# Kernel tuning notes

Measured on AMD Instinct MI355X. Metric: run time of the kernel, lower is better.

Reference implementation:

```python
import jax, jax.numpy as jnp
import numpy as np

EPS = 1e-5
NH = 8   # num_heads
P = 8    # patch_size (local window)

def layernorm(x, g, b):
    m = jnp.mean(x, axis=-1, keepdims=True)
    v = jnp.var(x, axis=-1, keepdims=True)
    return (x - m) * jax.lax.rsqrt(v + EPS) * g + b

def axis_embed(pos, nf):
    # DETR-style interleaved sin/cos along one axis -> (L, nf)
    dim_t = 10000.0 ** (2.0 * (jnp.arange(nf) // 2).astype(jnp.float32) / nf)
    p = pos[:, None] / dim_t
    return jnp.stack([jnp.sin(p[:, 0::2]), jnp.cos(p[:, 1::2])], axis=-1).reshape(pos.shape[0], nf)

def pos_embed_2d(E, H, W):
    # (H, W, E): first half of channels encode y, second half encode x
    half = E // 2
    ye = axis_embed(jnp.arange(1, H + 1, dtype=jnp.float32), half)
    xe = axis_embed(jnp.arange(1, W + 1, dtype=jnp.float32), half)
    return jnp.concatenate([jnp.broadcast_to(ye[:, None, :], (H, W, half)),
                            jnp.broadcast_to(xe[None, :, :], (H, W, half))], axis=-1)

def pos_embed_1d(L, E):
    # standard sinusoidal, (L, 1, E)
    pos = jnp.arange(L, dtype=jnp.float32)[:, None]
    div = jnp.exp(jnp.arange(0, E, 2, dtype=jnp.float32) * (-np.log(10000.0) / E))
    pe = jnp.zeros((L, E), jnp.float32)
    pe = pe.at[:, 0::2].set(jnp.sin(pos * div)).at[:, 1::2].set(jnp.cos(pos * div))
    return pe[:, None, :]

def mha(q, k, v, Wq, bq, Wk, bk, Wv, bv, Wo, bo, nh):
    # q,k,v: (B, L, C)
    B, Lq, C = q.shape
    hd = C // nh
    qh = (q @ Wq + bq).reshape(B, Lq, nh, hd)
    kh = (k @ Wk + bk).reshape(B, -1, nh, hd)
    vh = (v @ Wv + bv).reshape(B, -1, nh, hd)
    att = jax.nn.softmax(jnp.einsum('bqhd,bkhd->bhqk', qh, kh) / np.sqrt(hd).astype(np.float32), axis=-1)
    out = jnp.einsum('bhqk,bkhd->bqhd', att, vh).reshape(B, Lq, C)
    return out @ Wo + bo

def win_part(x):
    # (N,T,H,W,C) -> (N*T*nWin, P*P, C)
    N, T, H, W, C = x.shape
    x = x.reshape(N, T, H // P, P, W // P, P, C).transpose(0, 1, 2, 4, 3, 5, 6)
    return x.reshape(-1, P * P, C)

def forward(x, g1, b1, g2, b2, g3, b3, g4, b4,
            sWq, sbq, sWk, sbk, sWv, sbv, sWo, sbo,
            cW1, cb1, dwk, dwb, cW2, cb2,
            tWq, tbq, tWk, tbk, tWv, tbv, tWo, tbo,
            fW1, fb1, fW2, fb2):
    N, T, H, W, C = x.shape
    sl_pos = jnp.tile(pos_embed_2d(C, P, P), (H // P, W // P, 1))  # (H,W,C)
    tem_pos = pos_embed_1d(T, C)                                   # (T,1,C)

    # --- spatial local windowed MHSA (q=k=norm1(x+pos), v=norm1(x)) ---
    qk = win_part(layernorm(x + sl_pos, g1, b1))
    vv = win_part(layernorm(x, g1, b1))
    attn = mha(qk, qk, vv, sWq, sbq, sWk, sbk, sWv, sbv, sWo, sbo, NH)
    attn = attn.reshape(N, T, H // P, W // P, P, P, C).transpose(0, 1, 2, 4, 3, 5, 6).reshape(N, T, H, W, C)
    x = x + attn

    # --- Conv FFN: linear -> depthwise 3x3 -> GELU -> linear ---
    h = layernorm(x, g2, b2) @ cW1 + cb1
    Ch = h.shape[-1]
    h = h.reshape(N * T, H, W, Ch).transpose(0, 3, 1, 2)  # NCHW
    h = jax.lax.conv_general_dilated(h, dwk, (1, 1), 'SAME', feature_group_count=Ch,
                                     dimension_numbers=('NCHW', 'OIHW', 'NCHW')) + dwb[None, :, None, None]
    h = jax.nn.gelu(h, approximate=False)
    h = h.transpose(0, 2, 3, 1).reshape(N, T, H, W, Ch)
    x = x + (h @ cW2 + cb2)

    # --- temporal MHSA over T, tokens are (n,h,w) positions ---
    xt = x.transpose(1, 0, 2, 3, 4).reshape(T, N * H * W, C)
    xt = layernorm(xt, g3, b3)
    qt = layernorm(xt + tem_pos, g3, b3).transpose(1, 0, 2)  # (B,T,C)
    vt = layernorm(xt, g3, b3).transpose(1, 0, 2)
    xt = xt + mha(qt, qt, vt, tWq, tbq, tWk, tbk, tWv, tbv, tWo, tbo, NH).transpose(1, 0, 2)

    # --- FFN; original does x = x + drop3(x) (no residual, doubles output) ---
    xt = layernorm(xt, g4, b4)
    xt = jax.nn.gelu(xt @ fW1 + fb1, approximate=False) @ fW2 + fb2
    xt = xt + xt
    return xt.reshape(T, N, H, W, C).transpose(1, 0, 2, 3, 4)

def setup_inputs() -> dict:
    key = jax.random.key(0)
    N, T, H, W, C, DFF, HID = 4, 16, 32, 32, 256, 1024, 1024
    ks = iter(jax.random.split(key, 64))
    def w(*s):
        return jax.random.normal(next(ks), s, jnp.float32) * 0.02
    inp = dict(x=jax.random.normal(next(ks), (N, T, H, W, C), jnp.float32))
    for i in ('1', '2', '3', '4'):
        inp['g' + i] = jnp.ones((C,), jnp.float32)
        inp['b' + i] = jnp.zeros((C,), jnp.float32)
    for pfx in ('s', 't'):
        inp.update({pfx + 'Wq': w(C, C), pfx + 'bq': jnp.zeros((C,), jnp.float32),
                    pfx + 'Wk': w(C, C), pfx + 'bk': jnp.zeros((C,), jnp.float32),
                    pfx + 'Wv': w(C, C), pfx + 'bv': jnp.zeros((C,), jnp.float32),
                    pfx + 'Wo': w(C, C), pfx + 'bo': jnp.zeros((C,), jnp.float32)})
    inp.update(cW1=w(C, HID), cb1=jnp.zeros((HID,), jnp.float32),
               dwk=w(HID, 1, 3, 3), dwb=jnp.zeros((HID,), jnp.float32),
               cW2=w(HID, C), cb2=jnp.zeros((C,), jnp.float32))
    inp.update(fW1=w(C, DFF), fb1=jnp.zeros((DFF,), jnp.float32),
               fW2=w(DFF, C), fb2=jnp.zeros((C,), jnp.float32))
    return inp

def reference(x, g1, b1, g2, b2, g3, b3, g4, b4,
              sWq, sbq, sWk, sbk, sWv, sbv, sWo, sbo,
              cW1, cb1, dwk, dwb, cW2, cb2,
              tWq, tbq, tWk, tbk, tWv, tbv, tWo, tbo,
              fW1, fb1, fW2, fb2):
    return forward(x, g1, b1, g2, b2, g3, b3, g4, b4,
                   sWq, sbq, sWk, sbk, sWv, sbv, sWo, sbo,
                   cW1, cb1, dwk, dwb, cW2, cb2,
                   tWq, tbq, tWk, tbk, tWv, tbv, tWo, tbo,
                   fW1, fb1, fW2, fb2)
```

## Files before the change

kernel.cpp:

```cpp
#include <hip/hip_runtime.h>
#include <hip/hip_bf16.h>

typedef unsigned short u16;
typedef unsigned int u32;
typedef __attribute__((ext_vector_type(4))) float f32x4;
typedef __attribute__((ext_vector_type(8))) short s16x8;

static constexpr int Nn = 4, Tt = 16, Hh = 32, Ww = 32, Cc = 256;
static constexpr int Ltok = Nn * Tt * Hh * Ww;

__device__ __forceinline__ float bf2f(u16 v) {
  union { u32 u; float f; } t; t.u = ((u32)v) << 16; return t.f;
}
__device__ __forceinline__ u16 f2bf(float f) {
  union { u32 u; float f; } t; t.f = f;
  return (u16)((t.u + 0x7fffu + ((t.u >> 16) & 1u)) >> 16);
}
__device__ __forceinline__ ushort4 pack4(float a, float b, float c, float d) {
  ushort4 r; r.x = f2bf(a); r.y = f2bf(b); r.z = f2bf(c); r.w = f2bf(d); return r;
}
__device__ __forceinline__ float geluf(float x) {
  return 0.5f * x * (1.0f + erff(x * 0.70710678118654752f));
}
__device__ __forceinline__ float wsum(float v) {
#pragma unroll
  for (int o = 32; o > 0; o >>= 1) v += __shfl_xor(v, o, 64);
  return v;
}
__device__ __forceinline__ void ln_stats(float a0, float a1, float a2, float a3,
                                         float& m, float& inv) {
  float s  = wsum(a0 + a1 + a2 + a3);
  float s2 = wsum(a0 * a0 + a1 * a1 + a2 * a2 + a3 * a3);
  m = s * (1.0f / 256.0f);
  float v = s2 * (1.0f / 256.0f) - m * m;
  inv = rsqrtf(v + 1e-5f);
}
__device__ __forceinline__ void gload16(const u16* g, u16* l) {
  __builtin_amdgcn_global_load_lds(
      (const __attribute__((address_space(1))) void*)g,
      (__attribute__((address_space(3))) void*)l, 16, 0, 0);
}

__global__ __launch_bounds__(256) void k_pos(float* __restrict__ pe2d,
                                             float* __restrict__ pe1d,
                                             float* __restrict__ dwkT,
                                             float* __restrict__ zb,
                                             float* __restrict__ sqk,
                                             float* __restrict__ tqk,
                                             const float* __restrict__ dwk,
                                             const float* __restrict__ sbq,
                                             const float* __restrict__ sbk,
                                             const float* __restrict__ tbq,
                                             const float* __restrict__ tbk) {
  int idx = blockIdx.x * 256 + threadIdx.x;
  if (idx < 16384) {
    int y = idx >> 11, r = idx & 2047, x = r >> 8, c = r & 255;
    float pos; int cc;
    if (c < 128) { pos = (float)(y + 1); cc = c; }
    else         { pos = (float)(x + 1); cc = c - 128; }
    float e = (float)(cc & ~1) * (1.0f / 128.0f);
    float v = pos / powf(10000.0f, e);
    pe2d[idx] = (cc & 1) ? cosf(v) : sinf(v);
  } else if (idx < 20480) {
    int i = idx - 16384;
    int t = i >> 8, c = i & 255;
    float e = (float)(c & ~1) * (1.0f / 256.0f);
    float v = (float)t * powf(10000.0f, -e);
    pe1d[i] = (c & 1) ? cosf(v) : sinf(v);
  } else if (idx < 29696) {
    int i = idx - 20480;
    int c = i & 1023, tap = i >> 10;
    dwkT[tap * 1024 + c] = dwk[c * 9 + tap];
  } else if (idx < 30720) {
    zb[idx - 29696] = 0.0f;
  } else if (idx < 31232) {
    int i = idx - 30720;
    sqk[i] = (i < 256) ? sbq[i] : sbk[i - 256];
  } else if (idx < 31744) {
    int i = idx - 31232;
    tqk[i] = (i < 256) ? tbq[i] : tbk[i - 256];
  }
}

__global__ __launch_bounds__(256) void k_wprep(
    const float* __restrict__ s0, const float* __restrict__ s1,
    const float* __restrict__ s2, const float* __restrict__ s3,
    const float* __restrict__ s4, const float* __restrict__ s5,
    const float* __restrict__ s6, const float* __restrict__ s7,
    const float* __restrict__ cW1, const float* __restrict__ cW2,
    const float* __restrict__ fW1, const float* __restrict__ fW2,
    u16* __restrict__ WT) {
  __shared__ float Ls[32][33];
  int b = blockIdx.x;
// ... 52 lines not shown
  float m, inv;
  ln_stats(x0, x1, x2, x3, m, inv);
  float4 gv = *(const float4*)&g[c0];
  float4 bv = *(const float4*)&b[c0];
  *(ushort4*)&out[(size_t)l * Cc + c0] =
      pack4((x0 - m) * inv * gv.x + bv.x, (x1 - m) * inv * gv.y + bv.y,
            (x2 - m) * inv * gv.z + bv.z, (x3 - m) * inv * gv.w + bv.w);
}

__global__ __launch_bounds__(256) void k_ln3b(const u16* __restrict__ xa,
                                              const float* __restrict__ g,
                                              const float* __restrict__ b,
                                              const float* __restrict__ pe1d,
                                              u16* __restrict__ xt_base,
                                              u16* __restrict__ qt,
                                              u16* __restrict__ vt) {
  int l = blockIdx.x * 4 + (threadIdx.x >> 6);
  int lane = threadIdx.x & 63, c0 = lane * 4;
  ushort4 xv4 = *(const ushort4*)&xa[(size_t)l * Cc + c0];
  float x0 = bf2f(xv4.x), x1 = bf2f(xv4.y), x2 = bf2f(xv4.z), x3 = bf2f(xv4.w);
  float4 gv = *(const float4*)&g[c0];
  float4 bv = *(const float4*)&b[c0];
  float m, inv;
  ln_stats(x0, x1, x2, x3, m, inv);
  float t0 = (x0 - m) * inv * gv.x + bv.x;
  float t1 = (x1 - m) * inv * gv.y + bv.y;
  float t2 = (x2 - m) * inv * gv.z + bv.z;
  float t3 = (x3 - m) * inv * gv.w + bv.w;
  *(ushort4*)&xt_base[(size_t)l * Cc + c0] = pack4(t0, t1, t2, t3);
  float m2, inv2;
  ln_stats(t0, t1, t2, t3, m2, inv2);
  *(ushort4*)&vt[(size_t)l * Cc + c0] =
      pack4((t0 - m2) * inv2 * gv.x + bv.x, (t1 - m2) * inv2 * gv.y + bv.y,
            (t2 - m2) * inv2 * gv.z + bv.z, (t3 - m2) * inv2 * gv.w + bv.w);
  int tt = (l >> 10) & 15;
  float4 pv = *(const float4*)&pe1d[tt * Cc + c0];
  float s0 = t0 + pv.x, s1 = t1 + pv.y, s2 = t2 + pv.z, s3 = t3 + pv.w;
  float m3, inv3;
  ln_stats(s0, s1, s2, s3, m3, inv3);
  *(ushort4*)&qt[(size_t)l * Cc + c0] =
      pack4((s0 - m3) * inv3 * gv.x + bv.x, (s1 - m3) * inv3 * gv.y + bv.y,
            (s2 - m3) * inv3 * gv.z + bv.z, (s3 - m3) * inv3 * gv.w + bv.w);
}

template <int MODE>
__global__ __launch_bounds__(256, 2) void k_sgemm(const u16* __restrict__ A,
                                                  const u16* __restrict__ WT,
                                                  int wt_stride,
                                                  const float* __restrict__ bias,
                                                  int bias_stride,
                                                  const void* __restrict__ res,
                                                  void* __restrict__ out,
                                                  size_t out_xoff, int ldout) {
  __shared__ u16 SMEM[24576];
  const int tid = threadIdx.x;
  const int wave = tid >> 6, lane = tid & 63;
  const int fr = lane & 15, fs = lane >> 4;
  const int bx = blockIdx.x;
  const int r0base = blockIdx.y * 128;
  WT += (size_t)bx * wt_stride;
  bias += bx * bias_stride;
  u16* ob = (u16*)out + (size_t)bx * out_xoff;
  s16x8 wreg[4][8];
#pragma unroll
  for (int ni = 0; ni < 4; ++ni)
#pragma unroll
    for (int kt = 0; kt < 8; ++kt)
      wreg[ni][kt] = *(const s16x8*)&WT[(size_t)(wave * 64 + ni * 16 + fr) * 256 +
                                        kt * 32 + fs * 8];
  auto stage = [&](int buf, int r0) {
    u16* Ad = SMEM + buf * 8192;
#pragma unroll
    for (int i = 0; i < 4; ++i) {
      int idx = i * 256 + tid;
      int row = idx >> 5, s = idx & 31;
      gload16(A + (size_t)(r0 + row) * 256 + ((s ^ row) << 3), &Ad[idx * 8]);
    }
  };
  u16* sc = SMEM + 16384 + wave * 2048;
  stage(0, r0base);
  __syncthreads();
#pragma unroll 1
  for (int c = 0; c < 4; ++c) {
    if (c < 3) stage((c + 1) & 1, r0base + (c + 1) * 32);
    const u16* As = SMEM + (c & 1) * 8192;
    f32x4 acc[2][4] = {};
#pragma unroll
    for (int kt = 0; kt < 8; ++kt) {
      s16x8 a0 = *(const s16x8*)&As[(fr * 32 + ((kt * 4 + fs) ^ fr)) * 8];
      s16x8 a1 = *(const s16x8*)&As[((16 + fr) * 32 + ((kt * 4 + fs) ^ (16 + fr))) * 8];
#pragma unroll
      for (int ni = 0; ni < 4; ++ni) {
        acc[0][ni] = __builtin_amdgcn_mfma_f32_16x16x32_bf16(a0, wreg[ni][kt],
                                                             acc[0][ni], 0, 0, 0);
        acc[1][ni] = __builtin_amdgcn_mfma_f32_16x16x32_bf16(a1, wreg[ni][kt],
                                                             acc[1][ni], 0, 0, 0);
      }
    }
    const int r0 = r0base + c * 32;
    if constexpr (MODE == 5) {
      u16* o = (u16*)out;
#pragma unroll
      for (int ni = 0; ni < 4; ++ni) {
        int gc = wave * 64 + ni * 16 + fr;
        float bv = bias[gc];
#pragma unroll
        for (int mi = 0; mi < 2; ++mi) {
          int gr = r0 + mi * 16 + fs * 4;
          *(ushort4*)&o[(size_t)gc * (size_t)Ltok + gr] =
              pack4(acc[mi][ni][0] + bv, acc[mi][ni][1] + bv,
                    acc[mi][ni][2] + bv, acc[mi][ni][3] + bv);
        }
      }
    } else {
#pragma unroll
      for (int ni = 0; ni < 4; ++ni) {
        float bv = bias[wave * 64 + ni * 16 + fr];
#pragma unroll
        for (int mi = 0; mi < 2; ++mi)
#pragma unroll
          for (int r = 0; r < 4; ++r) {
            int row = mi * 16 + fs * 4 + r;
            int col = ni * 16 + fr;
            float v = acc[mi][ni][r] + bv;
            if constexpr (MODE == 1) v = geluf(v);
            sc[row * 64 + (col ^ ((row & 3) << 3))] = f2bf(v);
          }
      }
#pragma unroll
      for (int p = 0; p < 4; ++p) {
        int row = p * 8 + (lane >> 3);
        int c8 = (lane & 7) * 8;
        ushort4 u0 = *(const ushort4*)&sc[row * 64 + ((c8 ^ ((row & 3) << 3)))];
        ushort4 u1 = *(const ushort4*)&sc[row * 64 + (((c8 + 4) ^ ((row & 3) << 3)))];
        int gr = r0 + row;
        int gc = wave * 64 + c8;
        size_t o = (size_t)gr * (size_t)ldout + gc;
        if constexpr (MODE == 3) {
          const u16* rp = (const u16*)res;
          ushort4 r0v = *(const ushort4*)&rp[(size_t)gr * 256 + gc];
          ushort4 r1v = *(const ushort4*)&rp[(size_t)gr * 256 + gc + 4];
          u0 = pack4(bf2f(u0.x) + bf2f(r0v.x), bf2f(u0.y) + bf2f(r0v.y),
                     bf2f(u0.z) + bf2f(r0v.z), bf2f(u0.w) + bf2f(r0v.w));
          u1 = pack4(bf2f(u1.x) + bf2f(r1v.x), bf2f(u1.y) + bf2f(r1v.y),
                     bf2f(u1.z) + bf2f(r1v.z), bf2f(u1.w) + bf2f(r1v.w));
        }
        if constexpr (MODE == 7) {
          const float* rp = (const float*)res;
          float4 r0v = *(const float4*)&rp[(size_t)gr * 256 + gc];
          float4 r1v = *(const float4*)&rp[(size_t)gr * 256 + gc + 4];
          u0 = pack4(bf2f(u0.x) + r0v.x, bf2f(u0.y) + r0v.y,
                     bf2f(u0.z) + r0v.z, bf2f(u0.w) + r0v.w);
          u1 = pack4(bf2f(u1.x) + r1v.x, bf2f(u1.y) + r1v.y,
                     bf2f(u1.z) + r1v.z, bf2f(u1.w) + r1v.w);
        }
        *(ushort4*)&ob[o] = u0;
        *(ushort4*)&ob[o + 4] = u1;
      }
    }
    __syncthreads();
  }
}

__global__ __launch_bounds__(256, 2) void k_cgemm(const u16* __restrict__ A,
                                                  const u16* __restrict__ WT,
                                                  const float* __restrict__ bias,
                                                  u16* __restrict__ xa) {
  __shared__ u16 SMEM[18432];
  const int tid = threadIdx.x;
  const int wave = tid >> 6, lane = tid & 63;
  const int fr = lane & 15, fs = lane >> 4;
  const int bx = blockIdx.x;
  const int r0base = blockIdx.y * 128;
  s16x8 wreg[2][16];
#pragma unroll
  for (int ni = 0; ni < 2; ++ni)
#pragma unroll
    for (int kt = 0; kt < 16; ++kt)
      wreg[ni][kt] = *(const s16x8*)&WT[(size_t)(bx * 128 + wave * 32 + ni * 16 + fr) *
                                            1024 + kt * 32 + fs * 8];
  auto stage = [&](int buf, int r0) {
    u16* Ad = SMEM + buf * 8192;
#pragma unroll
    for (int i = 0; i < 4; ++i) {
      int idx = i * 256 + tid;
      int row = idx >> 6, s = idx & 63;
      gload16(A + (size_t)(r0 + row) * 512 + ((s ^ (row & 7)) << 3), &Ad[idx * 8]);
    }
  };
  u16* sc = SMEM + 16384 + wave * 512;
  stage(0, r0base);
  __syncthreads();
#pragma unroll 1
  for (int c = 0; c < 8; ++c) {
    if (c < 7) stage((c + 1) & 1, r0base + (c + 1) * 16);
    const u16* As = SMEM + (c & 1) * 8192;
    f32x4 acc[2] = {};
#pragma unroll
    for (int kt = 0; kt < 16; ++kt) {
      s16x8 a = *(const s16x8*)&As[fr * 512 + (((kt * 4 + fs) ^ (fr & 7)) << 3)];
#pragma unroll
      for (int ni = 0; ni < 2; ++ni)
        acc[ni] = __builtin_amdgcn_mfma_f32_16x16x32_bf16(a, wreg[ni][kt],
                                                          acc[ni], 0, 0, 0);
    }
    const int r0 = r0base + c * 16;
#pragma unroll
    for (int ni = 0; ni < 2; ++ni) {
      float bv = bias[bx * 128 + wave * 32 + ni * 16 + fr];
#pragma unroll
      for (int r = 0; r < 4; ++r) {
        int row = fs * 4 + r;
        int col = ni * 16 + fr;
        sc[row * 32 + (col ^ ((row & 3) << 3))] = f2bf(acc[ni][r] + bv);
      }
    }
    {
      int row = lane >> 2, c8 = (lane & 3) * 8;
      ushort4 u0 = *(const ushort4*)&sc[row * 32 + (c8 ^ ((row & 3) << 3))];
      ushort4 u1 = *(const ushort4*)&sc[row * 32 + ((c8 + 4) ^ ((row & 3) << 3))];
      int gr = r0 + row;
      int gc = bx * 128 + wave * 32 + c8;
      size_t o = (size_t)gr * 256 + gc;
      ushort4 r0v = *(const ushort4*)&xa[o];
      ushort4 r1v = *(const ushort4*)&xa[o + 4];
      *(ushort4*)&xa[o] = pack4(bf2f(u0.x) + bf2f(r0v.x), bf2f(u0.y) + bf2f(r0v.y),
                                bf2f(u0.z) + bf2f(r0v.z), bf2f(u0.w) + bf2f(r0v.w));
      *(ushort4*)&xa[o + 4] = pack4(bf2f(u1.x) + bf2f(r1v.x), bf2f(u1.y) + bf2f(r1v.y),
                                    bf2f(u1.z) + bf2f(r1v.z), bf2f(u1.w) + bf2f(r1v.w));
    }
    __syncthreads();
  }
}

__global__ __launch_bounds__(256, 2) void k_fgemm(const u16* __restrict__ A,
                                                  const u16* __restrict__ WT,
                                                  const float* __restrict__ bias,
                                                  float* __restrict__ out) {
  __shared__ u16 SMEM[34816];
  const int tid = threadIdx.x;
  const int wave = tid >> 6, lane = tid & 63;
  const int fr = lane & 15, fs = lane >> 4;
  const int bx = blockIdx.x;
  const int r0base = blockIdx.y * 128;
  const int col = bx * 64 + wave * 16 + fr;
  s16x8 wreg[32];
#pragma unroll
  for (int kt = 0; kt < 32; ++kt)
    wreg[kt] = *(const s16x8*)&WT[(size_t)col * 1024 + kt * 32 + fs * 8];
  auto stage = [&](int buf, int r0) {
    u16* Ad = SMEM + buf * 16384;
#pragma unroll
    for (int i = 0; i < 8; ++i) {
      int idx = i * 256 + tid;
      int row = idx >> 7, s = idx & 127;
      gload16(A + (size_t)(r0 + row) * 1024 + ((s ^ (row & 7)) << 3), &Ad[idx * 8]);
    }
  };
  float* scf = (float*)(SMEM + 32768) + wave * 256;
  stage(0, r0base);
  __syncthreads();
#pragma unroll 1
  for (int c = 0; c < 8; ++c) {
    if (c < 7) stage((c + 1) & 1, r0base + (c + 1) * 16);
    const u16* As = SMEM + (c & 1) * 16384;
    f32x4 acc = {};
#pragma unroll
    for (int kt = 0; kt < 32; ++kt) {
      s16x8 a = *(const s16x8*)&As[fr * 1024 + (((kt * 4 + fs) ^ (fr & 7)) << 3)];
      acc = __builtin_amdgcn_mfma_f32_16x16x32_bf16(a, wreg[kt], acc, 0, 0, 0);
    }
    const int r0 = r0base + c * 16;
    {
      float bv = bias[col];
#pragma unroll
      for (int r = 0; r < 4; ++r) {
        int row = fs * 4 + r;
        scf[row * 16 + (fr ^ ((row & 3) << 2))] = 2.0f * (acc[r] + bv);
      }
    }
    {
      int row = lane >> 2, c4 = (lane & 3) * 4;
      f32x4 v4 = *(const f32x4*)&scf[row * 16 + (c4 ^ ((row & 3) << 2))];
      int gr = r0 + row;
      *(float4*)&out[(size_t)gr * 256 + bx * 64 + wave * 16 + c4] =
          make_float4(v4[0], v4[1], v4[2], v4[3]);
    }
    __syncthreads();
  }
}

__global__ __launch_bounds__(256) void k_sattn2(const u16* __restrict__ Q,
                                                const u16* __restrict__ Kb,
                                                const u16* __restrict__ VT,
                                                u16* __restrict__ ctx) {
  __shared__ u16 P_lds[4][4096];
  const int tid = threadIdx.x;
  const int wave = tid >> 6, lane = tid & 63;
  const int fr = lane & 15, fs = lane >> 4;
  const int wi = blockIdx.x >> 1;
  const int head = (blockIdx.x & 1) * 4 + wave;
  const int ft = wi >> 4, wy = (wi >> 2) & 3, wx = wi & 3;
  const int base = ft * 1024 + wy * 256 + wx * 8;
  const float scale = 0.17677669529663688f;
  const int ch = head * 32 + fs * 8;
  s16x8 ka[4], qb[4];
#pragma unroll
  for (int t4 = 0; t4 < 4; ++t4) {
    int tok = base + (2 * t4 + (fr >> 3)) * 32 + (fr & 7);
    ka[t4] = *(const s16x8*)&Kb[(size_t)tok * 256 + ch];
    qb[t4] = *(const s16x8*)&Q[(size_t)tok * 256 + ch];
  }
  f32x4 s[4][4] = {};
#pragma unroll
  for (int kt = 0; kt < 4; ++kt)
#pragma unroll
    for (int qt = 0; qt < 4; ++qt)
      s[kt][qt] = __builtin_amdgcn_mfma_f32_16x16x32_bf16(ka[kt], qb[qt], s[kt][qt], 0, 0, 0);
  u16* pw = P_lds[wave];
#pragma unroll
  for (int qt = 0; qt < 4; ++qt) {
    float m = -1e30f;
#pragma unroll
    for (int kt = 0; kt < 4; ++kt)
#pragma unroll
      for (int r = 0; r < 4; ++r) m = fmaxf(m, s[kt][qt][r]);
    m = fmaxf(m, __shfl_xor(m, 16, 64));
    m = fmaxf(m, __shfl_xor(m, 32, 64));
    m *= scale;
    float e[4][4];
    float sum = 0.f;
#pragma unroll
    for (int kt = 0; kt < 4; ++kt)
#pragma unroll
      for (int r = 0; r < 4; ++r) {
        e[kt][r] = __expf(s[kt][qt][r] * scale - m);
        sum += e[kt][r];
      }
    sum += __shfl_xor(sum, 16, 64);
    sum += __shfl_xor(sum, 32, 64);
    float il = 1.0f / sum;
// ... 123 lines not shown
      const u16* hp = (const u16*)&hv;
      int tap = (ky + 1) * 3 + (kx + 1);
      float wk[8];
      *(float4*)&wk[0] = *(const float4*)&dwkT[tap * 1024 + tc0];
      *(float4*)&wk[4] = *(const float4*)&dwkT[tap * 1024 + tc0 + 4];
#pragma unroll
      for (int u = 0; u < 8; ++u) acc[u] = fmaf(bf2f(hp[u]), wk[u], acc[u]);
    }
  }
  size_t ob = (size_t)l * 512 + oco + c0;
  *(ushort4*)&Hout[ob] = pack4(geluf(acc[0]), geluf(acc[1]), geluf(acc[2]), geluf(acc[3]));
  *(ushort4*)&Hout[ob + 4] = pack4(geluf(acc[4]), geluf(acc[5]), geluf(acc[6]), geluf(acc[7]));
}

extern "C" void kernel_launch(void* const* d_in, const int* in_sizes, int n_in,
                              void* d_out, int out_size, void* d_ws, size_t ws_size,
                              hipStream_t stream) {
  (void)in_sizes; (void)n_in; (void)out_size; (void)ws_size;
  const float* x   = (const float*)d_in[0];
  const float* g1  = (const float*)d_in[1];  const float* b1  = (const float*)d_in[2];
  const float* g2  = (const float*)d_in[3];  const float* b2  = (const float*)d_in[4];
  const float* g3  = (const float*)d_in[5];  const float* b3  = (const float*)d_in[6];
  const float* g4  = (const float*)d_in[7];  const float* b4  = (const float*)d_in[8];
  const float* sWq = (const float*)d_in[9];  const float* sbq = (const float*)d_in[10];
  const float* sWk = (const float*)d_in[11]; const float* sbk = (const float*)d_in[12];
  const float* sWv = (const float*)d_in[13]; const float* sbv = (const float*)d_in[14];
  const float* sWo = (const float*)d_in[15]; const float* sbo = (const float*)d_in[16];
  const float* tWq = (const float*)d_in[17]; const float* tbq = (const float*)d_in[18];
  const float* tWk = (const float*)d_in[19]; const float* tbk = (const float*)d_in[20];
  const float* tWv = (const float*)d_in[21]; const float* tbv = (const float*)d_in[22];
  const float* tWo = (const float*)d_in[23]; const float* tbo = (const float*)d_in[24];
  const float* cW1 = (const float*)d_in[25]; const float* cb1 = (const float*)d_in[26];
  const float* dwk = (const float*)d_in[27]; const float* dwb = (const float*)d_in[28];
  const float* cW2 = (const float*)d_in[29]; const float* cb2 = (const float*)d_in[30];
  const float* fW1 = (const float*)d_in[31]; const float* fb1 = (const float*)d_in[32];
  const float* fW2 = (const float*)d_in[33]; const float* fb2 = (const float*)d_in[34];

  char* ws = (char*)d_ws;
  const size_t MB = 1ull << 20;
  float* PE2D = (float*)(ws);
  float* PE1D = (float*)(ws + (64 << 10));
  float* DWKT = (float*)(ws + (80 << 10));
  float* ZB   = (float*)(ws + (116 << 10));
  float* SQK  = (float*)(ws + (120 << 10));
  float* TQK  = (float*)(ws + (122 << 10));
  u16*   WT   = (u16*)(ws + (128 << 10));
  u16* XA  = (u16*)(ws + 4 * MB);
  u16* X1  = (u16*)(ws + 4 * MB);
  u16* H1A = (u16*)(ws + 36 * MB);
  u16* B1  = (u16*)(ws + 68 * MB);
  u16* B2  = (u16*)(ws + 100 * MB);
  u16* B3  = (u16*)(ws + 132 * MB);
  u16* B4  = (u16*)(ws + 164 * MB);
  u16* H1B = B4;
  u16* H2h = B2;
  u16* F1  = (u16*)(ws + 4 * MB);

  u16* sWqT = WT;
  u16* sWvT = WT + 2 * 65536;   u16* sWoT = WT + 3 * 65536;
  u16* tWqT = WT + 4 * 65536;
  u16* tWvT = WT + 6 * 65536;   u16* tWoT = WT + 7 * 65536;
  u16* cW1T = WT + 524288;      u16* cW2T = WT + 786432;
  u16* fW1T = WT + 1048576;     u16* fW2T = WT + 1310720;

  dim3 blk(256);
  dim3 gLN(Ltok / 4);

  k_pos<<<dim3(124), blk, 0, stream>>>(PE2D, PE1D, DWKT, ZB, SQK, TQK,
                                       dwk, sbq, sbk, tbq, tbk);
  k_wprep<<<dim3(1536), blk, 0, stream>>>(sWq, sWk, sWv, sWo, tWq, tWk, tWv, tWo,
                                          cW1, cW2, fW1, fW2, WT);
  k_ln1<<<gLN, blk, 0, stream>>>(x, g1, b1, PE2D, B1, B2);
  k_sgemm<5><<<dim3(1, 512), blk, 0, stream>>>(B2, sWvT, 0, sbv, 0, nullptr,
                                               B3, 0, 0);
  k_sgemm<0><<<dim3(2, 512), blk, 0, stream>>>(B1, sWqT, 65536, SQK, 256, nullptr,
                                               B2, 33554432ull, 256);
  k_sattn2<<<dim3(2048), blk, 0, stream>>>(B2, B4, B3, B1);
  k_sgemm<7><<<dim3(1, 512), blk, 0, stream>>>(B1, sWoT, 0, sbo, 0, x,
                                               XA, 0, 256);
  k_lnb<<<gLN, blk, 0, stream>>>(XA, g2, b2, B1);
  for (int h = 0; h < 2; ++h) {
    k_sgemm<0><<<dim3(2, 512), blk, 0, stream>>>(B1, cW1T + h * 2 * 65536, 65536,
                                                 cb1 + h * 512, 256, nullptr,
                                                 H1A, 67108864ull, 256);
    k_dwconv<<<dim3(Ltok * 32 / 256), blk, 0, stream>>>(H1A, DWKT, dwb,
                                                        (h * 2) * 256, 0, H2h);
    k_dwconv<<<dim3(Ltok * 32 / 256), blk, 0, stream>>>(H1B, DWKT, dwb,
                                                        (h * 2 + 1) * 256, 256, H2h);
    k_cgemm<<<dim3(2, 512), blk, 0, stream>>>(H2h, cW2T + h * 512,
                                              h ? cb2 : ZB, XA);
  }
  k_ln3b<<<gLN, blk, 0, stream>>>(XA, g3, b3, PE1D, B1, B2, B3);
  k_sgemm<0><<<dim3(1, 512), blk, 0, stream>>>(B3, tWvT, 0, tbv, 0, nullptr,
                                               B4, 0, 256);
  k_sgemm<0><<<dim3(2, 512), blk, 0, stream>>>(B2, tWqT, 65536, TQK, 256, nullptr,
                                               X1, 67108864ull, 256);
  k_tattn2<<<dim3(4096), blk, 0, stream>>>(X1, B3, B4, B2);
  k_sgemm<3><<<dim3(1, 512), blk, 0, stream>>>(B2, tWoT, 0, tbo, 0, B1,
                                               B3, 0, 256);
  k_lnb<<<gLN, blk, 0, stream>>>(B3, g4, b4, B4);
  k_sgemm<1><<<dim3(4, 512), blk, 0, stream>>>(B4, fW1T, 65536, fb1, 256, nullptr,
                                               F1, 256ull, 1024);
  k_fgemm<<<dim3(4, 512), blk, 0, stream>>>(F1, fW2T, fb2, (float*)d_out);
}
```

Measured before the change: 794.6 us.

## Load GEMM A-fragments directly from global into registers instead of LDS staging

The three GEMM kernels (k_sgemm, k_cgemm, k_fgemm) stop staging A tiles into shared memory with global_load_lds and block-wide barriers. Each wave now loads its 16-row A fragments straight into registers, ping-ponging between two register buffers so the next tile's loads overlap the current tile's MFMAs. The only shared memory left is a small per-wave scratch for the output transpose. k_cgemm is also retiled to 64 output columns per block, doubling its grid. This removes LDS traffic and __syncthreads, but each wave now fetches the same rows redundantly from global/L2, and register pressure rises, which may hurt occupancy.

```diff
diff --git a/kernel.cpp b/kernel.cpp
--- a/kernel.cpp
+++ b/kernel.cpp
@@ -34,11 +34,6 @@
   m = s * (1.0f / 256.0f);
   float v = s2 * (1.0f / 256.0f) - m * m;
   inv = rsqrtf(v + 1e-5f);
-}
-__device__ __forceinline__ void gload16(const u16* g, u16* l) {
-  __builtin_amdgcn_global_load_lds(
-      (const __attribute__((address_space(1))) void*)g,
-      (__attribute__((address_space(3))) void*)l, 16, 0, 0);
 }
 
 __global__ __launch_bounds__(256) void k_pos(float* __restrict__ pe2d,
@@ -197,7 +192,7 @@
                                                   const void* __restrict__ res,
                                                   void* __restrict__ out,
                                                   size_t out_xoff, int ldout) {
-  __shared__ u16 SMEM[24576];
+  __shared__ u16 SC[4][1024];
   const int tid = threadIdx.x;
   const int wave = tid >> 6, lane = tid & 63;
   const int fr = lane & 15, fs = lane >> 4;
@@ -213,97 +208,88 @@
     for (int kt = 0; kt < 8; ++kt)
       wreg[ni][kt] = *(const s16x8*)&WT[(size_t)(wave * 64 + ni * 16 + fr) * 256 +
                                         kt * 32 + fs * 8];
-  auto stage = [&](int buf, int r0) {
-    u16* Ad = SMEM + buf * 8192;
-#pragma unroll
-    for (int i = 0; i < 4; ++i) {
-      int idx = i * 256 + tid;
-      int row = idx >> 5, s = idx & 31;
-      gload16(A + (size_t)(r0 + row) * 256 + ((s ^ row) << 3), &Ad[idx * 8]);
-    }
+  const u16* Arow = A + (size_t)(r0base + fr) * 256 + fs * 8;
+  u16* sc = SC[wave];
+
+  s16x8 afA[8], afB[8];
+  auto lda = [&](s16x8* af, int t) {
+#pragma unroll
+    for (int kt = 0; kt < 8; ++kt)
+      af[kt] = *(const s16x8*)(Arow + t * 4096 + kt * 32);
   };
-  u16* sc = SMEM + 16384 + wave * 2048;
-  stage(0, r0base);
-  __syncthreads();
-#pragma unroll 1
-  for (int c = 0; c < 4; ++c) {
-    if (c < 3) stage((c + 1) & 1, r0base + (c + 1) * 32);
-    const u16* As = SMEM + (c & 1) * 8192;
-    f32x4 acc[2][4] = {};
-#pragma unroll
-    for (int kt = 0; kt < 8; ++kt) {
-      s16x8 a0 = *(const s16x8*)&As[(fr * 32 + ((kt * 4 + fs) ^ fr)) * 8];
-      s16x8 a1 = *(const s16x8*)&As[((16 + fr) * 32 + ((kt * 4 + fs) ^ (16 + fr))) * 8];
-#pragma unroll
-      for (int ni = 0; ni < 4; ++ni) {
-        acc[0][ni] = __builtin_amdgcn_mfma_f32_16x16x32_bf16(a0, wreg[ni][kt],
-                                                             acc[0][ni], 0, 0, 0);
-        acc[1][ni] = __builtin_amdgcn_mfma_f32_16x16x32_bf16(a1, wreg[ni][kt],
-                                                             acc[1][ni], 0, 0, 0);
-      }
-    }
-    const int r0 = r0base + c * 32;
+  auto work = [&](const s16x8* af, int t) {
+    f32x4 acc[4] = {};
+#pragma unroll
+    for (int kt = 0; kt < 8; ++kt)
+#pragma unroll
+      for (int ni = 0; ni < 4; ++ni)
+        acc[ni] = __builtin_amdgcn_mfma_f32_16x16x32_bf16(af[kt], wreg[ni][kt],
+                                                          acc[ni], 0, 0, 0);
+    const int r0 = r0base + t * 16;
     if constexpr (MODE == 5) {
       u16* o = (u16*)out;
 #pragma unroll
       for (int ni = 0; ni < 4; ++ni) {
         int gc = wave * 64 + ni * 16 + fr;
         float bv = bias[gc];
-#pragma unroll
-        for (int mi = 0; mi < 2; ++mi) {
-          int gr = r0 + mi * 16 + fs * 4;
-          *(ushort4*)&o[(size_t)gc * (size_t)Ltok + gr] =
-              pack4(acc[mi][ni][0] + bv, acc[mi][ni][1] + bv,
-                    acc[mi][ni][2] + bv, acc[mi][ni][3] + bv);
-        }
+        int gr = r0 + fs * 4;
+        *(ushort4*)&o[(size_t)gc * (size_t)Ltok + gr] =
+            pack4(acc[ni][0] + bv, acc[ni][1] + bv, acc[ni][2] + bv, acc[ni][3] + bv);
       }
-    } else {
-#pragma unroll
-      for (int ni = 0; ni < 4; ++ni) {
-        float bv = bias[wave * 64 + ni * 16 + fr];
-#pragma unroll
-        for (int mi = 0; mi < 2; ++mi)
-#pragma unroll
-          for (int r = 0; r < 4; ++r) {
-            int row = mi * 16 + fs * 4 + r;
-            int col = ni * 16 + fr;
-            float v = acc[mi][ni][r] + bv;
-            if constexpr (MODE == 1) v = geluf(v);
-            sc[row * 64 + (col ^ ((row & 3) << 3))] = f2bf(v);
-          }
+      return;
+    }
+#pragma unroll
+    for (int ni = 0; ni < 4; ++ni) {
+      float bv = bias[wave * 64 + ni * 16 + fr];
+#pragma unroll
+      for (int r = 0; r < 4; ++r) {
+        int row = fs * 4 + r;
+        int col = ni * 16 + fr;
+        float v = acc[ni][r] + bv;
+        if constexpr (MODE == 1) v = geluf(v);
+        sc[row * 64 + (col ^ ((row & 3) << 3))] = f2bf(v);
       }
-#pragma unroll
-      for (int p = 0; p < 4; ++p) {
-        int row = p * 8 + (lane >> 3);
-        int c8 = (lane & 7) * 8;
-        ushort4 u0 = *(const ushort4*)&sc[row * 64 + ((c8 ^ ((row & 3) << 3)))];
-        ushort4 u1 = *(const ushort4*)&sc[row * 64 + (((c8 + 4) ^ ((row & 3) << 3)))];
-        int gr = r0 + row;
-        int gc = wave * 64 + c8;
-        size_t o = (size_t)gr * (size_t)ldout + gc;
-        if constexpr (MODE == 3) {
-          const u16* rp = (const u16*)res;
-          ushort4 r0v = *(const ushort4*)&rp[(size_t)gr * 256 + gc];
-          ushort4 r1v = *(const ushort4*)&rp[(size_t)gr * 256 + gc + 4];
-          u0 = pack4(bf2f(u0.x) + bf2f(r0v.x), bf2f(u0.y) + bf2f(r0v.y),
-                     bf2f(u0.z) + bf2f(r0v.z), bf2f(u0.w) + bf2f(r0v.w));
-          u1 = pack4(bf2f(u1.x) + bf2f(r1v.x), bf2f(u1.y) + bf2f(r1v.y),
-                     bf2f(u1.z) + bf2f(r1v.z), bf2f(u1.w) + bf2f(r1v.w));
-        }
-        if constexpr (MODE == 7) {
-          const float* rp = (const float*)res;
-          float4 r0v = *(const float4*)&rp[(size_t)gr * 256 + gc];
-          float4 r1v = *(const float4*)&rp[(size_t)gr * 256 + gc + 4];
-          u0 = pack4(bf2f(u0.x) + r0v.x, bf2f(u0.y) + r0v.y,
-                     bf2f(u0.z) + r0v.z, bf2f(u0.w) + r0v.w);
-          u1 = pack4(bf2f(u1.x) + r1v.x, bf2f(u1.y) + r1v.y,
-                     bf2f(u1.z) + r1v.z, bf2f(u1.w) + r1v.w);
-        }
-        *(ushort4*)&ob[o] = u0;
-        *(ushort4*)&ob[o + 4] = u1;
+    }
+#pragma unroll
+    for (int p = 0; p < 2; ++p) {
+      int row = p * 8 + (lane >> 3);
+      int c8 = (lane & 7) * 8;
+      uint4 u = *(const uint4*)&sc[row * 64 + (c8 ^ ((row & 3) << 3))];
+      int gr = r0 + row;
+      int gc = wave * 64 + c8;
+      size_t o = (size_t)gr * (size_t)ldout + gc;
+      if constexpr (MODE == 3) {
+        uint4 rv = *(const uint4*)&((const u16*)res)[(size_t)gr * 256 + gc];
+        const u16* up = (const u16*)&u;
+        const u16* rp = (const u16*)&rv;
+        u16 ov[8];
+#pragma unroll
+        for (int j = 0; j < 8; ++j) ov[j] = f2bf(bf2f(up[j]) + bf2f(rp[j]));
+        u = *(const uint4*)ov;
       }
-    }
-    __syncthreads();
+      if constexpr (MODE == 7) {
+        const float* rp = (const float*)res;
+        float4 r0v = *(const float4*)&rp[(size_t)gr * 256 + gc];
+        float4 r1v = *(const float4*)&rp[(size_t)gr * 256 + gc + 4];
+        const u16* up = (const u16*)&u;
+        u16 ov[8];
+        ov[0] = f2bf(bf2f(up[0]) + r0v.x); ov[1] = f2bf(bf2f(up[1]) + r0v.y);
+        ov[2] = f2bf(bf2f(up[2]) + r0v.z); ov[3] = f2bf(bf2f(up[3]) + r0v.w);
+        ov[4] = f2bf(bf2f(up[4]) + r1v.x); ov[5] = f2bf(bf2f(up[5]) + r1v.y);
+        ov[6] = f2bf(bf2f(up[6]) + r1v.z); ov[7] = f2bf(bf2f(up[7]) + r1v.w);
+        u = *(const uint4*)ov;
+      }
+      *(uint4*)&ob[o] = u;
+    }
+  };
+
+  lda(afA, 0);
+#pragma unroll
+  for (int tp = 0; tp < 4; ++tp) {
+    lda(afB, tp * 2 + 1);
+    work(afA, tp * 2);
+    if (tp < 3) lda(afA, tp * 2 + 2);
+    work(afB, tp * 2 + 1);
   }
 }
 
@@ -311,70 +297,57 @@
                                                   const u16* __restrict__ WT,
                                                   const float* __restrict__ bias,
                                                   u16* __restrict__ xa) {
-  __shared__ u16 SMEM[18432];
+  __shared__ u16 SC[4][256];
   const int tid = threadIdx.x;
   const int wave = tid >> 6, lane = tid & 63;
   const int fr = lane & 15, fs = lane >> 4;
   const int bx = blockIdx.x;
   const int r0base = blockIdx.y * 128;
-  s16x8 wreg[2][16];
-#pragma unroll
-  for (int ni = 0; ni < 2; ++ni)
+  const int col = bx * 64 + wave * 16 + fr;
+  s16x8 wreg[16];
+#pragma unroll
+  for (int kt = 0; kt < 16; ++kt)
+    wreg[kt] = *(const s16x8*)&WT[(size_t)col * 1024 + kt * 32 + fs * 8];
+  const u16* Arow = A + (size_t)(r0base + fr) * 512 + fs * 8;
+  u16* sc = SC[wave];
+  const float bv = bias[col];
+
+  s16x8 afA[16], afB[16];
+  auto lda = [&](s16x8* af, int t) {
 #pragma unroll
     for (int kt = 0; kt < 16; ++kt)
-      wreg[ni][kt] = *(const s16x8*)&WT[(size_t)(bx * 128 + wave * 32 + ni * 16 + fr) *
-                                            1024 + kt * 32 + fs * 8];
-  auto stage = [&](int buf, int r0) {
-    u16* Ad = SMEM + buf * 8192;
-#pragma unroll
-    for (int i = 0; i < 4; ++i) {
-      int idx = i * 256 + tid;
-      int row = idx >> 6, s = idx & 63;
-      gload16(A + (size_t)(r0 + row) * 512 + ((s ^ (row & 7)) << 3), &Ad[idx * 8]);
-    }
+      af[kt] = *(const s16x8*)(Arow + t * 8192 + kt * 32);
   };
-  u16* sc = SMEM + 16384 + wave * 512;
-  stage(0, r0base);
-  __syncthreads();
-#pragma unroll 1
-  for (int c = 0; c < 8; ++c) {
-    if (c < 7) stage((c + 1) & 1, r0base + (c + 1) * 16);
-    const u16* As = SMEM + (c & 1) * 8192;
-    f32x4 acc[2] = {};
-#pragma unroll
-    for (int kt = 0; kt < 16; ++kt) {
-      s16x8 a = *(const s16x8*)&As[fr * 512 + (((kt * 4 + fs) ^ (fr & 7)) << 3)];
-#pragma unroll
-      for (int ni = 0; ni < 2; ++ni)
-        acc[ni] = __builtin_amdgcn_mfma_f32_16x16x32_bf16(a, wreg[ni][kt],
-                                                          acc[ni], 0, 0, 0);
-    }
-    const int r0 = r0base + c * 16;
-#pragma unroll
-    for (int ni = 0; ni < 2; ++ni) {
-      float bv = bias[bx * 128 + wave * 32 + ni * 16 + fr];
-#pragma unroll
-      for (int r = 0; r < 4; ++r) {
-        int row = fs * 4 + r;
-        int col = ni * 16 + fr;
-        sc[row * 32 + (col ^ ((row & 3) << 3))] = f2bf(acc[ni][r] + bv);
-      }
+  auto work = [&](const s16x8* af, int t) {
+    f32x4 acc = {};
+#pragma unroll
+    for (int kt = 0; kt < 16; ++kt)
+      acc = __builtin_amdgcn_mfma_f32_16x16x32_bf16(af[kt], wreg[kt], acc, 0, 0, 0);
+    const int r0 = r0base + t * 16;
+#pragma unroll
+    for (int r = 0; r < 4; ++r) {
+      int row = fs * 4 + r;
+      sc[row * 16 + (fr ^ (((row >> 2) & 3) << 2))] = f2bf(acc[r] + bv);
     }
     {
-      int row = lane >> 2, c8 = (lane & 3) * 8;
-      ushort4 u0 = *(const ushort4*)&sc[row * 32 + (c8 ^ ((row & 3) << 3))];
-      ushort4 u1 = *(const ushort4*)&sc[row * 32 + ((c8 + 4) ^ ((row & 3) << 3))];
+      int row = lane >> 2, c4 = (lane & 3) * 4;
+      ushort4 u = *(const ushort4*)&sc[row * 16 + (c4 ^ (((row >> 2) & 3) << 2))];
       int gr = r0 + row;
-      int gc = bx * 128 + wave * 32 + c8;
+      int gc = bx * 64 + wave * 16 + c4;
       size_t o = (size_t)gr * 256 + gc;
-      ushort4 r0v = *(const ushort4*)&xa[o];
-      ushort4 r1v = *(const ushort4*)&xa[o + 4];
-      *(ushort4*)&xa[o] = pack4(bf2f(u0.x) + bf2f(r0v.x), bf2f(u0.y) + bf2f(r0v.y),
-                                bf2f(u0.z) + bf2f(r0v.z), bf2f(u0.w) + bf2f(r0v.w));
-      *(ushort4*)&xa[o + 4] = pack4(bf2f(u1.x) + bf2f(r1v.x), bf2f(u1.y) + bf2f(r1v.y),
-                                    bf2f(u1.z) + bf2f(r1v.z), bf2f(u1.w) + bf2f(r1v.w));
-    }
-    __syncthreads();
+      ushort4 rv = *(const ushort4*)&xa[o];
+      *(ushort4*)&xa[o] = pack4(bf2f(u.x) + bf2f(rv.x), bf2f(u.y) + bf2f(rv.y),
+                                bf2f(u.z) + bf2f(rv.z), bf2f(u.w) + bf2f(rv.w));
+    }
+  };
+
+  lda(afA, 0);
+#pragma unroll
+  for (int tp = 0; tp < 4; ++tp) {
+    lda(afB, tp * 2 + 1);
+    work(afA, tp * 2);
+    if (tp < 3) lda(afA, tp * 2 + 2);
+    work(afB, tp * 2 + 1);
   }
 }
 
@@ -382,7 +355,7 @@
                                                   const u16* __restrict__ WT,
                                                   const float* __restrict__ bias,
                                                   float* __restrict__ out) {
-  __shared__ u16 SMEM[34816];
+  __shared__ float SCF[4][256];
   const int tid = threadIdx.x;
   const int wave = tid >> 6, lane = tid & 63;
   const int fr = lane & 15, fs = lane >> 4;
@@ -393,45 +366,44 @@
 #pragma unroll
   for (int kt = 0; kt < 32; ++kt)
     wreg[kt] = *(const s16x8*)&WT[(size_t)col * 1024 + kt * 32 + fs * 8];
-  auto stage = [&](int buf, int r0) {
-    u16* Ad = SMEM + buf * 16384;
-#pragma unroll
-    for (int i = 0; i < 8; ++i) {
-      int idx = i * 256 + tid;
-      int row = idx >> 7, s = idx & 127;
-      gload16(A + (size_t)(r0 + row) * 1024 + ((s ^ (row & 7)) << 3), &Ad[idx * 8]);
-    }
+  const u16* Arow = A + (size_t)(r0base + fr) * 1024 + fs * 8;
+  float* sc = SCF[wave];
+  const float bv = bias[col];
+
+  s16x8 aA[8], aB[8];
+  auto ld8 = [&](s16x8* af, int t, int h) {
+#pragma unroll
+    for (int kt = 0; kt < 8; ++kt)
+      af[kt] = *(const s16x8*)(Arow + t * 16384 + (h * 8 + kt) * 32);
   };
-  float* scf = (float*)(SMEM + 32768) + wave * 256;
-  stage(0, r0base);
-  __syncthreads();
-#pragma unroll 1
-  for (int c = 0; c < 8; ++c) {
-    if (c < 7) stage((c + 1) & 1, r0base + (c + 1) * 16);
-    const u16* As = SMEM + (c & 1) * 16384;
+  auto m8 = [&](const s16x8* af, int h, f32x4& acc) {
+#pragma unroll
+    for (int kt = 0; kt < 8; ++kt)
+      acc = __builtin_amdgcn_mfma_f32_16x16x32_bf16(af[kt], wreg[h * 8 + kt],
+                                                    acc, 0, 0, 0);
+  };
+
+  ld8(aA, 0, 0);
+  for (int t = 0; t < 8; ++t) {
     f32x4 acc = {};
-#pragma unroll
-    for (int kt = 0; kt < 32; ++kt) {
-      s16x8 a = *(const s16x8*)&As[fr * 1024 + (((kt * 4 + fs) ^ (fr & 7)) << 3)];
-      acc = __builtin_amdgcn_mfma_f32_16x16x32_bf16(a, wreg[kt], acc, 0, 0, 0);
-    }
-    const int r0 = r0base + c * 16;
-    {
-      float bv = bias[col];
-#pragma unroll
-      for (int r = 0; r < 4; ++r) {
-        int row = fs * 4 + r;
-        scf[row * 16 + (fr ^ ((row & 3) << 2))] = 2.0f * (acc[r] + bv);
-      }
+    ld8(aB, t, 1); m8(aA, 0, acc);
+    ld8(aA, t, 2); m8(aB, 1, acc);
+    ld8(aB, t, 3); m8(aA, 2, acc);
+    if (t < 7) ld8(aA, t + 1, 0);
+    m8(aB, 3, acc);
+    const int r0 = r0base + t * 16;
+#pragma unroll
+    for (int r = 0; r < 4; ++r) {
+      int row = fs * 4 + r;
+      sc[row * 16 + (fr ^ (((row >> 2) & 3) << 2))] = 2.0f * (acc[r] + bv);
     }
     {
       int row = lane >> 2, c4 = (lane & 3) * 4;
-      f32x4 v4 = *(const f32x4*)&scf[row * 16 + (c4 ^ ((row & 3) << 2))];
+      f32x4 v4 = *(const f32x4*)&sc[row * 16 + (c4 ^ (((row >> 2) & 3) << 2))];
       int gr = r0 + row;
       *(float4*)&out[(size_t)gr * 256 + bx * 64 + wave * 16 + c4] =
           make_float4(v4[0], v4[1], v4[2], v4[3]);
     }
-    __syncthreads();
   }
 }
 
@@ -661,7 +633,6 @@
   u16* B2  = (u16*)(ws + 100 * MB);
   u16* B3  = (u16*)(ws + 132 * MB);
   u16* B4  = (u16*)(ws + 164 * MB);
-  u16* H1B = B4;
   u16* H2h = B2;
   u16* F1  = (u16*)(ws + 4 * MB);
 
@@ -694,9 +665,9 @@
                                                  H1A, 67108864ull, 256);
     k_dwconv<<<dim3(Ltok * 32 / 256), blk, 0, stream>>>(H1A, DWKT, dwb,
                                                         (h * 2) * 256, 0, H2h);
-    k_dwconv<<<dim3(Ltok * 32 / 256), blk, 0, stream>>>(H1B, DWKT, dwb,
+    k_dwconv<<<dim3(Ltok * 32 / 256), blk, 0, stream>>>(B4, DWKT, dwb,
                                                         (h * 2 + 1) * 256, 256, H2h);
-    k_cgemm<<<dim3(2, 512), blk, 0, stream>>>(H2h, cW2T + h * 512,
+    k_cgemm<<<dim3(4, 512), blk, 0, stream>>>(H2h, cW2T + h * 512,
                                               h ? cb2 : ZB, XA);
   }
   k_ln3b<<<gLN, blk, 0, stream>>>(XA, g3, b3, PE1D, B1, B2, B3);
```

Result: slower. 1.395 ms (+75.6%).

## Halve rows per GEMM block and split fgemm K staging to cut LDS use

Applied to the files above, without the earlier changes.

Each GEMM block now handles 64 rows instead of 128, and the grids double to 1024 row-blocks, giving more blocks to fill the GPU and shorter per-block tails. The FFN2 GEMM now stages A in half-K chunks of 512 columns with a persistent accumulator, which shrinks its shared-memory footprint from about 68 KB. The cgemm and fgemm swizzles change to a full-row XOR. The trade-off is that each block reloads its register-resident weights over fewer rows, so weight-load overhead per row doubles.

```diff
diff --git a/kernel.cpp b/kernel.cpp
--- a/kernel.cpp
+++ b/kernel.cpp
@@ -202,7 +202,7 @@
   const int wave = tid >> 6, lane = tid & 63;
   const int fr = lane & 15, fs = lane >> 4;
   const int bx = blockIdx.x;
-  const int r0base = blockIdx.y * 128;
+  const int r0base = blockIdx.y * 64;
   WT += (size_t)bx * wt_stride;
   bias += bx * bias_stride;
   u16* ob = (u16*)out + (size_t)bx * out_xoff;
@@ -213,21 +213,22 @@
     for (int kt = 0; kt < 8; ++kt)
       wreg[ni][kt] = *(const s16x8*)&WT[(size_t)(wave * 64 + ni * 16 + fr) * 256 +
                                         kt * 32 + fs * 8];
-  auto stage = [&](int buf, int r0) {
+  auto stage = [&](int buf, int c) {
     u16* Ad = SMEM + buf * 8192;
 #pragma unroll
     for (int i = 0; i < 4; ++i) {
       int idx = i * 256 + tid;
       int row = idx >> 5, s = idx & 31;
-      gload16(A + (size_t)(r0 + row) * 256 + ((s ^ row) << 3), &Ad[idx * 8]);
+      gload16(A + (size_t)(r0base + c * 32 + row) * 256 + ((s ^ row) << 3),
+              &Ad[idx * 8]);
     }
   };
   u16* sc = SMEM + 16384 + wave * 2048;
-  stage(0, r0base);
+  stage(0, 0);
   __syncthreads();
 #pragma unroll 1
-  for (int c = 0; c < 4; ++c) {
-    if (c < 3) stage((c + 1) & 1, r0base + (c + 1) * 32);
+  for (int c = 0; c < 2; ++c) {
+    if (c < 1) stage(1, 1);
     const u16* As = SMEM + (c & 1) * 8192;
     f32x4 acc[2][4] = {};
 #pragma unroll
@@ -316,7 +317,7 @@
   const int wave = tid >> 6, lane = tid & 63;
   const int fr = lane & 15, fs = lane >> 4;
   const int bx = blockIdx.x;
-  const int r0base = blockIdx.y * 128;
+  const int r0base = blockIdx.y * 64;
   s16x8 wreg[2][16];
 #pragma unroll
   for (int ni = 0; ni < 2; ++ni)
@@ -324,26 +325,27 @@
     for (int kt = 0; kt < 16; ++kt)
       wreg[ni][kt] = *(const s16x8*)&WT[(size_t)(bx * 128 + wave * 32 + ni * 16 + fr) *
                                             1024 + kt * 32 + fs * 8];
-  auto stage = [&](int buf, int r0) {
+  auto stage = [&](int buf, int c) {
     u16* Ad = SMEM + buf * 8192;
 #pragma unroll
     for (int i = 0; i < 4; ++i) {
       int idx = i * 256 + tid;
       int row = idx >> 6, s = idx & 63;
-      gload16(A + (size_t)(r0 + row) * 512 + ((s ^ (row & 7)) << 3), &Ad[idx * 8]);
+      gload16(A + (size_t)(r0base + c * 16 + row) * 512 + ((s ^ row) << 3),
+              &Ad[idx * 8]);
     }
   };
   u16* sc = SMEM + 16384 + wave * 512;
-  stage(0, r0base);
+  stage(0, 0);
   __syncthreads();
 #pragma unroll 1
-  for (int c = 0; c < 8; ++c) {
-    if (c < 7) stage((c + 1) & 1, r0base + (c + 1) * 16);
+  for (int c = 0; c < 4; ++c) {
+    if (c < 3) stage((c + 1) & 1, c + 1);
     const u16* As = SMEM + (c & 1) * 8192;
     f32x4 acc[2] = {};
 #pragma unroll
     for (int kt = 0; kt < 16; ++kt) {
-      s16x8 a = *(const s16x8*)&As[fr * 512 + (((kt * 4 + fs) ^ (fr & 7)) << 3)];
+      s16x8 a = *(const s16x8*)&As[(fr * 64 + ((kt * 4 + fs) ^ fr)) * 8];
 #pragma unroll
       for (int ni = 0; ni < 2; ++ni)
         acc[ni] = __builtin_amdgcn_mfma_f32_16x16x32_bf16(a, wreg[ni][kt],
@@ -382,54 +384,59 @@
                                                   const u16* __restrict__ WT,
                                                   const float* __restrict__ bias,
                                                   float* __restrict__ out) {
-  __shared__ u16 SMEM[34816];
+  __shared__ u16 AB[2][8192];
+  __shared__ float SCF[4][256];
   const int tid = threadIdx.x;
   const int wave = tid >> 6, lane = tid & 63;
   const int fr = lane & 15, fs = lane >> 4;
   const int bx = blockIdx.x;
-  const int r0base = blockIdx.y * 128;
+  const int r0base = blockIdx.y * 64;
   const int col = bx * 64 + wave * 16 + fr;
   s16x8 wreg[32];
 #pragma unroll
   for (int kt = 0; kt < 32; ++kt)
     wreg[kt] = *(const s16x8*)&WT[(size_t)col * 1024 + kt * 32 + fs * 8];
-  auto stage = [&](int buf, int r0) {
-    u16* Ad = SMEM + buf * 16384;
-#pragma unroll
-    for (int i = 0; i < 8; ++i) {
+  const float bv = bias[col];
+  float* sc = SCF[wave];
+
+  auto stage = [&](int buf, int s) {
+    int t = s >> 1, h = s & 1;
+#pragma unroll
+    for (int i = 0; i < 4; ++i) {
       int idx = i * 256 + tid;
-      int row = idx >> 7, s = idx & 127;
-      gload16(A + (size_t)(r0 + row) * 1024 + ((s ^ (row & 7)) << 3), &Ad[idx * 8]);
+      int row = idx >> 6, ss = idx & 63;
+      gload16(A + (size_t)(r0base + t * 16 + row) * 1024 + h * 512 + ((ss ^ row) << 3),
+              &AB[buf][idx * 8]);
     }
   };
-  float* scf = (float*)(SMEM + 32768) + wave * 256;
-  stage(0, r0base);
+  stage(0, 0);
   __syncthreads();
+  f32x4 acc = {};
 #pragma unroll 1
-  for (int c = 0; c < 8; ++c) {
-    if (c < 7) stage((c + 1) & 1, r0base + (c + 1) * 16);
-    const u16* As = SMEM + (c & 1) * 16384;
-    f32x4 acc = {};
-#pragma unroll
-    for (int kt = 0; kt < 32; ++kt) {
-      s16x8 a = *(const s16x8*)&As[fr * 1024 + (((kt * 4 + fs) ^ (fr & 7)) << 3)];
-      acc = __builtin_amdgcn_mfma_f32_16x16x32_bf16(a, wreg[kt], acc, 0, 0, 0);
-    }
-    const int r0 = r0base + c * 16;
-    {
-      float bv = bias[col];
+  for (int s = 0; s < 8; ++s) {
+    if (s < 7) stage((s + 1) & 1, s + 1);
+    const u16* As = AB[s & 1];
+    const int h = s & 1;
+#pragma unroll
+    for (int kt = 0; kt < 16; ++kt) {
+      s16x8 a = *(const s16x8*)&As[(fr * 64 + ((kt * 4 + fs) ^ fr)) * 8];
+      acc = __builtin_amdgcn_mfma_f32_16x16x32_bf16(a, wreg[h * 16 + kt], acc, 0, 0, 0);
+    }
+    if (h) {
+      const int r0 = r0base + (s >> 1) * 16;
 #pragma unroll
       for (int r = 0; r < 4; ++r) {
         int row = fs * 4 + r;
-        scf[row * 16 + (fr ^ ((row & 3) << 2))] = 2.0f * (acc[r] + bv);
-      }
-    }
-    {
-      int row = lane >> 2, c4 = (lane & 3) * 4;
-      f32x4 v4 = *(const f32x4*)&scf[row * 16 + (c4 ^ ((row & 3) << 2))];
-      int gr = r0 + row;
-      *(float4*)&out[(size_t)gr * 256 + bx * 64 + wave * 16 + c4] =
-          make_float4(v4[0], v4[1], v4[2], v4[3]);
+        sc[row * 16 + (fr ^ ((row & 3) << 2))] = 2.0f * (acc[r] + bv);
+      }
+      {
+        int row = lane >> 2, c4 = (lane & 3) * 4;
+        f32x4 v4 = *(const f32x4*)&sc[row * 16 + (c4 ^ ((row & 3) << 2))];
+        int gr = r0 + row;
+        *(float4*)&out[(size_t)gr * 256 + bx * 64 + wave * 16 + c4] =
+            make_float4(v4[0], v4[1], v4[2], v4[3]);
+      }
+      acc = f32x4{0.f, 0.f, 0.f, 0.f};
     }
     __syncthreads();
   }
@@ -661,7 +668,6 @@
   u16* B2  = (u16*)(ws + 100 * MB);
   u16* B3  = (u16*)(ws + 132 * MB);
   u16* B4  = (u16*)(ws + 164 * MB);
-  u16* H1B = B4;
   u16* H2h = B2;
   u16* F1  = (u16*)(ws + 4 * MB);
 
@@ -680,35 +686,35 @@
   k_wprep<<<dim3(1536), blk, 0, stream>>>(sWq, sWk, sWv, sWo, tWq, tWk, tWv, tWo,
                                           cW1, cW2, fW1, fW2, WT);
   k_ln1<<<gLN, blk, 0, stream>>>(x, g1, b1, PE2D, B1, B2);
-  k_sgemm<5><<<dim3(1, 512), blk, 0, stream>>>(B2, sWvT, 0, sbv, 0, nullptr,
-                                               B3, 0, 0);
-  k_sgemm<0><<<dim3(2, 512), blk, 0, stream>>>(B1, sWqT, 65536, SQK, 256, nullptr,
-                                               B2, 33554432ull, 256);
+  k_sgemm<5><<<dim3(1, 1024), blk, 0, stream>>>(B2, sWvT, 0, sbv, 0, nullptr,
+                                                B3, 0, 0);
+  k_sgemm<0><<<dim3(2, 1024), blk, 0, stream>>>(B1, sWqT, 65536, SQK, 256, nullptr,
+                                                B2, 33554432ull, 256);
   k_sattn2<<<dim3(2048), blk, 0, stream>>>(B2, B4, B3, B1);
-  k_sgemm<7><<<dim3(1, 512), blk, 0, stream>>>(B1, sWoT, 0, sbo, 0, x,
-                                               XA, 0, 256);
+  k_sgemm<7><<<dim3(1, 1024), blk, 0, stream>>>(B1, sWoT, 0, sbo, 0, x,
+                                                XA, 0, 256);
   k_lnb<<<gLN, blk, 0, stream>>>(XA, g2, b2, B1);
   for (int h = 0; h < 2; ++h) {
-    k_sgemm<0><<<dim3(2, 512), blk, 0, stream>>>(B1, cW1T + h * 2 * 65536, 65536,
-                                                 cb1 + h * 512, 256, nullptr,
-                                                 H1A, 67108864ull, 256);
+    k_sgemm<0><<<dim3(2, 1024), blk, 0, stream>>>(B1, cW1T + h * 2 * 65536, 65536,
+                                                  cb1 + h * 512, 256, nullptr,
+                                                  H1A, 67108864ull, 256);
     k_dwconv<<<dim3(Ltok * 32 / 256), blk, 0, stream>>>(H1A, DWKT, dwb,
                                                         (h * 2) * 256, 0, H2h);
-    k_dwconv<<<dim3(Ltok * 32 / 256), blk, 0, stream>>>(H1B, DWKT, dwb,
+    k_dwconv<<<dim3(Ltok * 32 / 256), blk, 0, stream>>>(B4, DWKT, dwb,
                                                         (h * 2 + 1) * 256, 256, H2h);
-    k_cgemm<<<dim3(2, 512), blk, 0, stream>>>(H2h, cW2T + h * 512,
-                                              h ? cb2 : ZB, XA);
+    k_cgemm<<<dim3(2, 1024), blk, 0, stream>>>(H2h, cW2T + h * 512,
+                                               h ? cb2 : ZB, XA);
   }
   k_ln3b<<<gLN, blk, 0, stream>>>(XA, g3, b3, PE1D, B1, B2, B3);
-  k_sgemm<0><<<dim3(1, 512), blk, 0, stream>>>(B3, tWvT, 0, tbv, 0, nullptr,
-                                               B4, 0, 256);
-  k_sgemm<0><<<dim3(2, 512), blk, 0, stream>>>(B2, tWqT, 65536, TQK, 256, nullptr,
-                                               X1, 67108864ull, 256);
+  k_sgemm<0><<<dim3(1, 1024), blk, 0, stream>>>(B3, tWvT, 0, tbv, 0, nullptr,
+                                                B4, 0, 256);
+  k_sgemm<0><<<dim3(2, 1024), blk, 0, stream>>>(B2, tWqT, 65536, TQK, 256, nullptr,
+                                                X1, 67108864ull, 256);
   k_tattn2<<<dim3(4096), blk, 0, stream>>>(X1, B3, B4, B2);
-  k_sgemm<3><<<dim3(1, 512), blk, 0, stream>>>(B2, tWoT, 0, tbo, 0, B1,
-                                               B3, 0, 256);
+  k_sgemm<3><<<dim3(1, 1024), blk, 0, stream>>>(B2, tWoT, 0, tbo, 0, B1,
+                                                B3, 0, 256);
   k_lnb<<<gLN, blk, 0, stream>>>(B3, g4, b4, B4);
-  k_sgemm<1><<<dim3(4, 512), blk, 0, stream>>>(B4, fW1T, 65536, fb1, 256, nullptr,
-                                               F1, 256ull, 1024);
-  k_fgemm<<<dim3(4, 512), blk, 0, stream>>>(F1, fW2T, fb2, (float*)d_out);
-}
+  k_sgemm<1><<<dim3(4, 1024), blk, 0, stream>>>(B4, fW1T, 65536, fb1, 256, nullptr,
+                                                F1, 256ull, 1024);
+  k_fgemm<<<dim3(4, 1024), blk, 0, stream>>>(F1, fW2T, fb2, (float*)d_out);
+}
```

New measurement: 1.201 ms. 51.1% more time.
